# Kernel tuning notes

Measured on AMD Instinct MI355X. Metric: run time of the kernel, lower is better.

## Reference

```python
import jax, jax.numpy as jnp
import numpy as np

HEAD_DIM = 64
N_HEADS = 32
N_KV_HEADS = 8
ROPE_THETA = 10000.0
NEG_INF = -1e9


def _rope_cos_sin(position_ids, head_dim, dtype):
    # position_ids: [b, s] int -> cos/sin [b, s, head_dim]
    inv_freq = 1.0 / (ROPE_THETA ** (jnp.arange(0, head_dim, 2, dtype=jnp.float32) / head_dim))
    freqs = position_ids.astype(jnp.float32)[..., None] * inv_freq  # [b, s, d/2]
    emb = jnp.concatenate([freqs, freqs], axis=-1)                  # [b, s, d]
    return jnp.cos(emb).astype(dtype), jnp.sin(emb).astype(dtype)


def _rotate_half(x):
    half = x.shape[-1] // 2
    return jnp.concatenate([-x[..., half:], x[..., :half]], axis=-1)


def setup_inputs() -> dict:
    key = jax.random.key(0)
    ks = jax.random.split(key, 6)
    b, s, din = 2, 2048, 4096  # din = 2 * hidden_size
    hidden_states = jax.random.normal(ks[0], (b, s, din), dtype=jnp.float32)
    # additive causal mask [b, 1, q, kv]
    causal = jnp.tril(jnp.ones((s, s), dtype=bool))
    attention_mask = jnp.where(causal, 0.0, NEG_INF).astype(jnp.float32)
    attention_mask = jnp.broadcast_to(attention_mask[None, None], (b, 1, s, s))
    position_ids = jnp.broadcast_to(jnp.arange(s, dtype=jnp.int32)[None], (b, s))
    scale = 0.02
    Wq = jax.random.normal(ks[1], (din, N_HEADS * HEAD_DIM), dtype=jnp.float32) * scale
    Wk = jax.random.normal(ks[2], (din, N_KV_HEADS * HEAD_DIM), dtype=jnp.float32) * scale
    Wv = jax.random.normal(ks[3], (din, N_KV_HEADS * HEAD_DIM), dtype=jnp.float32) * scale
    Wo = jax.random.normal(ks[4], (N_HEADS * HEAD_DIM, din // 2), dtype=jnp.float32) * scale
    return {"hidden_states": hidden_states, "attention_mask": attention_mask,
            "position_ids": position_ids, "Wq": Wq, "Wk": Wk, "Wv": Wv, "Wo": Wo}


def reference(hidden_states, attention_mask, position_ids, Wq, Wk, Wv, Wo):
    b, s, _ = hidden_states.shape
    g = N_HEADS // N_KV_HEADS  # GQA group size
    q = (hidden_states @ Wq).reshape(b, s, N_HEADS, HEAD_DIM).transpose(0, 2, 1, 3)      # [b,h,s,d]
    k = (hidden_states @ Wk).reshape(b, s, N_KV_HEADS, HEAD_DIM).transpose(0, 2, 1, 3)   # [b,kh,s,d]
    v = (hidden_states @ Wv).reshape(b, s, N_KV_HEADS, HEAD_DIM).transpose(0, 2, 1, 3)
    cos, sin = _rope_cos_sin(position_ids, HEAD_DIM, q.dtype)  # [b,s,d]
    cos, sin = cos[:, None], sin[:, None]                      # [b,1,s,d]
    q = q * cos + _rotate_half(q) * sin
    k = k * cos + _rotate_half(k) * sin
    # GQA: group query heads instead of materializing repeated K/V
    qg = q.reshape(b, N_KV_HEADS, g, s, HEAD_DIM)
    scores = jnp.einsum('bhgqd,bhkd->bhgqk', qg, k) / jnp.sqrt(jnp.float32(HEAD_DIM))
    scores = scores + attention_mask[:, :, None]               # broadcast over kv-head, group
    probs = jax.nn.softmax(scores.astype(jnp.float32), axis=-1).astype(q.dtype)
    out = jnp.einsum('bhgqk,bhkd->bhgqd', probs, v)            # [b,kh,g,s,d]
    out = out.reshape(b, N_HEADS, s, HEAD_DIM).transpose(0, 2, 1, 3).reshape(b, s, N_HEADS * HEAD_DIM)
    return out @ Wo
```

## Files before the change

### kernel.cpp

```cpp
#include <hip/hip_runtime.h>
#include <hip/hip_bf16.h>
#include <cstdint>
#include <cstddef>

typedef __attribute__((ext_vector_type(4))) float floatx4;
typedef __attribute__((ext_vector_type(8))) short shortx8;

typedef __attribute__((address_space(1))) void gvoid;
typedef __attribute__((address_space(3))) void lvoid;

__device__ inline __hip_bfloat16 f2b(float x) { return __float2bfloat16(x); }
__device__ inline float b2f(__hip_bfloat16 x) { return __bfloat162float(x); }
__device__ inline unsigned cvt_pk_bf16(float lo, float hi) {
  unsigned r;
  asm("v_cvt_pk_bf16_f32 %0, %1, %2" : "=v"(r) : "v"(lo), "v"(hi));
  return r;
}
__device__ inline unsigned vmov(unsigned a) {
  unsigned r; asm("v_mov_b32 %0, %1" : "=v"(r) : "v"(a)); return r;
}
__device__ inline void plswap16(unsigned &a, unsigned &b) {
  asm("v_permlane16_swap_b32 %0, %1" : "+v"(a), "+v"(b));
}
__device__ inline void plswap32(unsigned &a, unsigned &b) {
  asm("v_permlane32_swap_b32 %0, %1" : "+v"(a), "+v"(b));
}
__device__ inline float red4_sum(float v) {
  unsigned a = __float_as_uint(v), b = vmov(a);
  plswap16(a, b);
  float s = __uint_as_float(a) + __uint_as_float(b);
  a = __float_as_uint(s); b = vmov(a);
  plswap32(a, b);
  return __uint_as_float(a) + __uint_as_float(b);
}

template <typename T> __device__ inline T cvt_out(float x);
template <> __device__ inline float cvt_out<float>(float x) { return x; }
template <> __device__ inline __hip_bfloat16 cvt_out<__hip_bfloat16>(float x) { return __float2bfloat16(x); }

__global__ void cvt_f32_bf16(const float* __restrict__ in, __hip_bfloat16* __restrict__ out, int n) {
  int i = (blockIdx.x * blockDim.x + threadIdx.x) * 4;
  if (i >= n) return;
  float4 v = *(const float4*)(in + i);
  __hip_bfloat16 o[4] = { f2b(v.x), f2b(v.y), f2b(v.z), f2b(v.w) };
  *(ushort4*)(out + i) = *(const ushort4*)o;
}

__global__ void transpose_cvt(const float* __restrict__ in, __hip_bfloat16* __restrict__ out, int K, int N) {
  __shared__ float tile[32][33];
  int n0 = blockIdx.x * 32, k0 = blockIdx.y * 32;
  int tx = threadIdx.x, ty = threadIdx.y;
#pragma unroll
  for (int i = 0; i < 4; i++)
    tile[ty + i * 8][tx] = in[(size_t)(k0 + ty + i * 8) * N + n0 + tx];
  __syncthreads();
#pragma unroll
  for (int i = 0; i < 4; i++)
    out[(size_t)(n0 + ty + i * 8) * K + k0 + tx] = f2b(tile[tx][ty + i * 8]);
}

template <typename OutT>
__global__ __launch_bounds__(256) void gemm_bt(
    const __hip_bfloat16* __restrict__ A,
    const __hip_bfloat16* __restrict__ Bt,
    OutT* __restrict__ C, int M, int N, int K) {
  __shared__ short lA[128 * 32];
  __shared__ short lB[128 * 32];
  const int m0 = blockIdx.x * 128, n0 = blockIdx.y * 128;
  const int t = threadIdx.x;
  const int l = t & 63;
  const int w = t >> 6;
  const int wm = (w & 1) * 64, wn = (w >> 1) * 64;
  const int lr = l & 15, lq = l >> 4;
  floatx4 acc[4][4] = {};

  for (int kt = 0; kt < K; kt += 32) {
    __syncthreads();
#pragma unroll
    for (int j = 0; j < 2; j++) {
      int flat = j * 2048 + t * 8;
      const __hip_bfloat16* srcA = A + (size_t)(m0 + (flat >> 5)) * K + kt + (flat & 31);
      __builtin_amdgcn_global_load_lds((gvoid*)srcA, (lvoid*)&lA[flat], 16, 0, 0);
      const __hip_bfloat16* srcB = Bt + (size_t)(n0 + (flat >> 5)) * K + kt + (flat & 31);
      __builtin_amdgcn_global_load_lds((gvoid*)srcB, (lvoid*)&lB[flat], 16, 0, 0);
    }
    __syncthreads();
    shortx8 af[4], bfr[4];
#pragma unroll
    for (int mi = 0; mi < 4; mi++)
      af[mi] = *(const shortx8*)&lA[(wm + mi * 16 + lr) * 32 + lq * 8];
#pragma unroll
    for (int ni = 0; ni < 4; ni++)
      bfr[ni] = *(const shortx8*)&lB[(wn + ni * 16 + lr) * 32 + lq * 8];
#pragma unroll
    for (int mi = 0; mi < 4; mi++)
#pragma unroll
      for (int ni = 0; ni < 4; ni++)
        acc[mi][ni] = __builtin_amdgcn_mfma_f32_16x16x32_bf16(af[mi], bfr[ni], acc[mi][ni], 0, 0, 0);
  }
#pragma unroll
  for (int mi = 0; mi < 4; mi++)
#pragma unroll
    for (int ni = 0; ni < 4; ni++) {
      int row = m0 + wm + mi * 16 + lq * 4;
      int col = n0 + wn + ni * 16 + lr;
#pragma unroll
      for (int r = 0; r < 4; r++)
        C[(size_t)(row + r) * N + col] = cvt_out<OutT>(acc[mi][ni][r]);
    }
}

__global__ void rope_kernel(__hip_bfloat16* __restrict__ q, int stride, float scale) {
  int i = threadIdx.x;
  int row = blockIdx.x * 8 + threadIdx.y;
  int head = blockIdx.y;
  int pos = row & 2047;
  float freq = (float)pos * exp2f(-(float)i * (13.287712379549449f / 32.0f));
  float s = sinf(freq), c = cosf(freq);
  __hip_bfloat16* p = q + (size_t)row * stride + head * 64 + i;
  float x1 = b2f(p[0]), x2 = b2f(p[32]);
  p[0]  = f2b((x1 * c - x2 * s) * scale);
  p[32] = f2b((x2 * c + x1 * s) * scale);
}

__global__ void v_transpose(const __hip_bfloat16* __restrict__ QKV, __hip_bfloat16* __restrict__ Vt) {
  __shared__ __hip_bfloat16 tile[32][33];
  int bkvh = blockIdx.z;
  int s0 = blockIdx.x * 32, d0 = blockIdx.y * 32;
  int b = bkvh >> 3, kvh = bkvh & 7;
  int tx = threadIdx.x, ty = threadIdx.y;
#pragma unroll
  for (int i = 0; i < 4; i++)
    tile[ty + i * 8][tx] = QKV[(size_t)(b * 2048 + s0 + ty + i * 8) * 3072 + 2560 + kvh * 64 + d0 + tx];
  __syncthreads();
#pragma unroll
  for (int i = 0; i < 4; i++)
    Vt[((size_t)(bkvh * 64 + d0 + ty + i * 8) << 11) + s0 + tx] = tile[tx][ty + i * 8];
}

__global__ __launch_bounds__(256, 3) void attn_kernel(
    const __hip_bfloat16* __restrict__ Qp,
    const __hip_bfloat16* __restrict__ Kp,
    const __hip_bfloat16* __restrict__ Vt,
    __hip_bfloat16* __restrict__ O) {
  __shared__ __align__(16) short lK[2][64 * 64];
  __shared__ __align__(16) short lV[2][64 * 64];
  const int h = blockIdx.y, b = blockIdx.z;
  const int ia = ((int)blockIdx.x + (h & 15) + ((h >> 4) << 3) + (b << 2)) & 15;
  const int ib = 31 - ia;
  const int kvh = h >> 2;
  const int t = threadIdx.x, w = t >> 6, l = t & 63;
  const int lr = l & 15, lq = l >> 4;
  const int swz = lr & 7;

  const int q0A = ia * 64 + w * 16;
  const int q0B = ib * 64 + w * 16;
  const __hip_bfloat16* qpA = Qp + (size_t)(b * 2048 + q0A + lr) * 3072 + h * 64 + lq * 8;
  const __hip_bfloat16* qpB = Qp + (size_t)(b * 2048 + q0B + lr) * 3072 + h * 64 + lq * 8;
  shortx8 qfA0 = *(const shortx8*)(qpA);
  shortx8 qfA1 = *(const shortx8*)(qpA + 32);
  shortx8 qfB0 = *(const shortx8*)(qpB);
  shortx8 qfB1 = *(const shortx8*)(qpB + 32);

  const int srow = t >> 3, schunk = t & 7;
  const int swzch = schunk ^ (srow & 7);
  const __hip_bfloat16* ksrc = Kp + (size_t)(b * 2048 + srow) * 3072 + kvh * 64 + swzch * 8;
  const __hip_bfloat16* vsrc = Vt + ((size_t)((b * 8 + kvh) * 64 + srow) << 11) + swzch * 8;

  floatx4 oA[4] = {}, oB[4] = {};
  float sumA = 0.f, sumB = 0.f;

  const int KT = 32 - ia;

  auto stage = [&](int sbuf, int kt2) {
#pragma unroll
    for (int j = 0; j < 2; j++) {
      __builtin_amdgcn_global_load_lds((gvoid*)(ksrc + (size_t)(kt2 * 64 + j * 32) * 3072),
                                       (lvoid*)&lK[sbuf][w * 512 + j * 2048], 16, 0, 0);
      __builtin_amdgcn_global_load_lds((gvoid*)(vsrc + (size_t)(j * 32) * 2048 + kt2 * 64),
                                       (lvoid*)&lV[sbuf][w * 512 + j * 2048], 16, 0, 0);
    }
  };

  stage(0, 0);

  for (int kt = 0; kt < KT; kt++) {
    const int buf = kt & 1;
    __syncthreads();
    if (kt + 1 < KT) stage(buf ^ 1, kt + 1);
    const bool doA = (kt <= ia);

    floatx4 sA[4] = {}, sB[4] = {};
    __builtin_amdgcn_s_setprio(1);
#pragma unroll
    for (int mi = 0; mi < 4; mi++) {
      const short* kr = &lK[buf][(mi * 16 + lr) * 64];
      shortx8 kf0 = *(const shortx8*)(kr + ((lq ^ swz) << 3));
      shortx8 kf1 = *(const shortx8*)(kr + (((4 + lq) ^ swz) << 3));
      if (doA) {
        sA[mi] = __builtin_amdgcn_mfma_f32_16x16x32_bf16(kf0, qfA0, sA[mi], 0, 0, 0);
        sA[mi] = __builtin_amdgcn_mfma_f32_16x16x32_bf16(kf1, qfA1, sA[mi], 0, 0, 0);
      }
      sB[mi] = __builtin_amdgcn_mfma_f32_16x16x32_bf16(kf0, qfB0, sB[mi], 0, 0, 0);
      sB[mi] = __builtin_amdgcn_mfma_f32_16x16x32_bf16(kf1, qfB1, sB[mi], 0, 0, 0);
    }
    __builtin_amdgcn_s_setprio(0);

    shortx8 pA0, pA1, pB0, pB1;

    if (doA) {
      if (kt == ia) {
#pragma unroll
        for (int mi = 0; mi < 4; mi++)
#pragma unroll
          for (int r = 0; r < 4; r++)
            if (mi * 16 + lq * 4 + r > w * 16 + lr) sA[mi][r] = -3e8f;
      }
      float rs = 0.f;
#pragma unroll
      for (int mi = 0; mi < 4; mi++) {
        float p0 = exp2f(sA[mi][0]), p1 = exp2f(sA[mi][1]);
        float p2 = exp2f(sA[mi][2]), p3 = exp2f(sA[mi][3]);
        sA[mi][0] = p0; sA[mi][1] = p1; sA[mi][2] = p2; sA[mi][3] = p3;
        rs += (p0 + p1) + (p2 + p3);
      }
      sumA += rs;
      unsigned Wm[4][2];
#pragma unroll
      for (int mi = 0; mi < 4; mi++) {
        Wm[mi][0] = cvt_pk_bf16(sA[mi][0], sA[mi][1]);
        Wm[mi][1] = cvt_pk_bf16(sA[mi][2], sA[mi][3]);
      }
      unsigned x0 = Wm[0][0], y0 = Wm[1][0]; plswap32(x0, y0); plswap16(x0, y0);
      unsigned x1 = Wm[0][1], y1 = Wm[1][1]; plswap32(x1, y1); plswap16(x1, y1);
      uint4 t0{x0, x1, y0, y1}; pA0 = *(const shortx8*)&t0;
      unsigned x2 = Wm[2][0], y2 = Wm[3][0]; plswap32(x2, y2); plswap16(x2, y2);
      unsigned x3 = Wm[2][1], y3 = Wm[3][1]; plswap32(x3, y3); plswap16(x3, y3);
      uint4 t1{x2, x3, y2, y3}; pA1 = *(const shortx8*)&t1;
    }

    {
      if (kt == KT - 1) {
#pragma unroll
        for (int mi = 0; mi < 4; mi++)
#pragma unroll
          for (int r = 0; r < 4; r++)
            if (mi * 16 + lq * 4 + r > w * 16 + lr) sB[mi][r] = -3e8f;
      }
      float rs = 0.f;
#pragma unroll
      for (int mi = 0; mi < 4; mi++) {
        float p0 = exp2f(sB[mi][0]), p1 = exp2f(sB[mi][1]);
        float p2 = exp2f(sB[mi][2]), p3 = exp2f(sB[mi][3]);
        sB[mi][0] = p0; sB[mi][1] = p1; sB[mi][2] = p2; sB[mi][3] = p3;
        rs += (p0 + p1) + (p2 + p3);
      }
      sumB += rs;
      unsigned Wm[4][2];
#pragma unroll
      for (int mi = 0; mi < 4; mi++) {
        Wm[mi][0] = cvt_pk_bf16(sB[mi][0], sB[mi][1]);
        Wm[mi][1] = cvt_pk_bf16(sB[mi][2], sB[mi][3]);
      }
      unsigned x0 = Wm[0][0], y0 = Wm[1][0]; plswap32(x0, y0); plswap16(x0, y0);
      unsigned x1 = Wm[0][1], y1 = Wm[1][1]; plswap32(x1, y1); plswap16(x1, y1);
      uint4 t0{x0, x1, y0, y1}; pB0 = *(const shortx8*)&t0;
      unsigned x2 = Wm[2][0], y2 = Wm[3][0]; plswap32(x2, y2); plswap16(x2, y2);
      unsigned x3 = Wm[2][1], y3 = Wm[3][1]; plswap32(x3, y3); plswap16(x3, y3);
      uint4 t1{x2, x3, y2, y3}; pB1 = *(const shortx8*)&t1;
    }

    __builtin_amdgcn_s_setprio(1);
#pragma unroll
    for (int mi = 0; mi < 4; mi++) {
      const short* vr = &lV[buf][(mi * 16 + lr) * 64];
      shortx8 vf0 = *(const shortx8*)(vr + ((lq ^ swz) << 3));
      shortx8 vf1 = *(const shortx8*)(vr + (((4 + lq) ^ swz) << 3));
      if (doA) {
        floatx4 o = oA[mi];
        o = __builtin_amdgcn_mfma_f32_16x16x32_bf16(vf0, pA0, o, 0, 0, 0);
        o = __builtin_amdgcn_mfma_f32_16x16x32_bf16(vf1, pA1, o, 0, 0, 0);
        oA[mi] = o;
      }
      floatx4 o2 = oB[mi];
      o2 = __builtin_amdgcn_mfma_f32_16x16x32_bf16(vf0, pB0, o2, 0, 0, 0);
      o2 = __builtin_amdgcn_mfma_f32_16x16x32_bf16(vf1, pB1, o2, 0, 0, 0);
      oB[mi] = o2;
    }
    __builtin_amdgcn_s_setprio(0);
  }

  const float livA = 1.f / red4_sum(sumA), livB = 1.f / red4_sum(sumB);
  __hip_bfloat16* obase = O + (size_t)(b * 2048 + q0A + lr) * 2048 + h * 64 + lq * 4;
#pragma unroll
  for (int mi = 0; mi < 4; mi++) {
    uint2 pk;
    pk.x = cvt_pk_bf16(oA[mi][0] * livA, oA[mi][1] * livA);
    pk.y = cvt_pk_bf16(oA[mi][2] * livA, oA[mi][3] * livA);
    *(uint2*)(obase + mi * 16) = pk;
  }
  __hip_bfloat16* obase2 = O + (size_t)(b * 2048 + q0B + lr) * 2048 + h * 64 + lq * 4;
#pragma unroll
  for (int mi = 0; mi < 4; mi++) {
    uint2 pk;
    pk.x = cvt_pk_bf16(oB[mi][0] * livB, oB[mi][1] * livB);
    pk.y = cvt_pk_bf16(oB[mi][2] * livB, oB[mi][3] * livB);
    *(uint2*)(obase2 + mi * 16) = pk;
  }
}

extern "C" void kernel_launch(void* const* d_in, const int* in_sizes, int n_in,
                              void* d_out, int out_size, void* d_ws, size_t ws_size,
                              hipStream_t stream) {
  (void)in_sizes; (void)n_in; (void)out_size; (void)ws_size;
  const float* hs = (const float*)d_in[0];
  const float* Wq = (const float*)d_in[3];
  const float* Wk = (const float*)d_in[4];
  const float* Wv = (const float*)d_in[5];
  const float* Wo = (const float*)d_in[6];
  float* out = (float*)d_out;

  char* p = (char*)d_ws;
  auto alloc = [&](size_t elts) { __hip_bfloat16* r = (__hip_bfloat16*)p; p += elts * 2; return r; };
  __hip_bfloat16* Xb   = alloc(4096ull * 4096);
  __hip_bfloat16* Wt   = alloc(3072ull * 4096);
  __hip_bfloat16* Wot  = alloc(2048ull * 2048);
  __hip_bfloat16* QKVb = alloc(4096ull * 3072);
  __hip_bfloat16* Vtb  = alloc(2ull * 8 * 64 * 2048);
  __hip_bfloat16* Ab   = alloc(4096ull * 2048);

  cvt_f32_bf16<<<16384, 256, 0, stream>>>(hs, Xb, 4096 * 4096);
  transpose_cvt<<<dim3(64, 128), dim3(32, 8), 0, stream>>>(Wq, Wt, 4096, 2048);
  transpose_cvt<<<dim3(16, 128), dim3(32, 8), 0, stream>>>(Wk, Wt + 2048ull * 4096, 4096, 512);
  transpose_cvt<<<dim3(16, 128), dim3(32, 8), 0, stream>>>(Wv, Wt + 2560ull * 4096, 4096, 512);
  transpose_cvt<<<dim3(64, 64), dim3(32, 8), 0, stream>>>(Wo, Wot, 2048, 2048);

  gemm_bt<__hip_bfloat16><<<dim3(32, 24), 256, 0, stream>>>(Xb, Wt, QKVb, 4096, 3072, 4096);

  rope_kernel<<<dim3(512, 32), dim3(32, 8), 0, stream>>>(QKVb, 3072, 0.18033688011112042f);
  rope_kernel<<<dim3(512, 8), dim3(32, 8), 0, stream>>>(QKVb + 2048, 3072, 1.0f);
  v_transpose<<<dim3(64, 2, 16), dim3(32, 8), 0, stream>>>(QKVb, Vtb);

  attn_kernel<<<dim3(16, 32, 2), 256, 0, stream>>>(QKVb, QKVb + 2048, Vtb, Ab);

  gemm_bt<float><<<dim3(32, 16), 256, 0, stream>>>(Ab, Wot, out, 4096, 2048, 2048);
}
```

Before: 492.4 us.

## Double-buffer GEMM LDS tiles with K=64 steps and XOR-swizzled layout

Rewrites the bf16 GEMM used for the QKV and output projections. K-tiles grow to 64, the LDS buffers are doubled so the next tile's global-to-LDS load overlaps the current tile's MFMAs, and LDS columns are XOR-swizzled to avoid bank conflicts. It also drops one barrier per iteration and raises wave priority around the MFMA block. LDS use grows to 64 KB per block, which may limit occupancy despite the launch bound of 2.

```diff
diff --git a/kernel.cpp b/kernel.cpp
--- a/kernel.cpp
+++ b/kernel.cpp
@@ -60,12 +60,12 @@
 }
 
 template <typename OutT>
-__global__ __launch_bounds__(256) void gemm_bt(
+__global__ __launch_bounds__(256, 2) void gemm_bt64(
     const __hip_bfloat16* __restrict__ A,
     const __hip_bfloat16* __restrict__ Bt,
     OutT* __restrict__ C, int M, int N, int K) {
-  __shared__ short lA[128 * 32];
-  __shared__ short lB[128 * 32];
+  __shared__ __align__(16) short lA[2][128 * 64];
+  __shared__ __align__(16) short lB[2][128 * 64];
   const int m0 = blockIdx.x * 128, n0 = blockIdx.y * 128;
   const int t = threadIdx.x;
   const int l = t & 63;
@@ -74,29 +74,48 @@
   const int lr = l & 15, lq = l >> 4;
   floatx4 acc[4][4] = {};
 
-  for (int kt = 0; kt < K; kt += 32) {
+  const int srow = t >> 3;
+  const int sc = (t & 7) ^ (srow & 7);
+  const __hip_bfloat16* aSrc = A + (size_t)(m0 + srow) * K + sc * 8;
+  const __hip_bfloat16* bSrc = Bt + (size_t)(n0 + srow) * K + sc * 8;
+
+  auto stage = [&](int sbuf, int kt) {
+#pragma unroll
+    for (int j = 0; j < 4; j++) {
+      __builtin_amdgcn_global_load_lds((gvoid*)(aSrc + (size_t)(j * 32) * K + kt),
+                                       (lvoid*)&lA[sbuf][t * 8 + j * 2048], 16, 0, 0);
+      __builtin_amdgcn_global_load_lds((gvoid*)(bSrc + (size_t)(j * 32) * K + kt),
+                                       (lvoid*)&lB[sbuf][t * 8 + j * 2048], 16, 0, 0);
+    }
+  };
+
+  stage(0, 0);
+  int buf = 0;
+  for (int kt = 0; kt < K; kt += 64) {
     __syncthreads();
-#pragma unroll
-    for (int j = 0; j < 2; j++) {
-      int flat = j * 2048 + t * 8;
-      const __hip_bfloat16* srcA = A + (size_t)(m0 + (flat >> 5)) * K + kt + (flat & 31);
-      __builtin_amdgcn_global_load_lds((gvoid*)srcA, (lvoid*)&lA[flat], 16, 0, 0);
-      const __hip_bfloat16* srcB = Bt + (size_t)(n0 + (flat >> 5)) * K + kt + (flat & 31);
-      __builtin_amdgcn_global_load_lds((gvoid*)srcB, (lvoid*)&lB[flat], 16, 0, 0);
-    }
-    __syncthreads();
-    shortx8 af[4], bfr[4];
-#pragma unroll
-    for (int mi = 0; mi < 4; mi++)
-      af[mi] = *(const shortx8*)&lA[(wm + mi * 16 + lr) * 32 + lq * 8];
-#pragma unroll
-    for (int ni = 0; ni < 4; ni++)
-      bfr[ni] = *(const shortx8*)&lB[(wn + ni * 16 + lr) * 32 + lq * 8];
-#pragma unroll
-    for (int mi = 0; mi < 4; mi++)
-#pragma unroll
-      for (int ni = 0; ni < 4; ni++)
-        acc[mi][ni] = __builtin_amdgcn_mfma_f32_16x16x32_bf16(af[mi], bfr[ni], acc[mi][ni], 0, 0, 0);
+    if (kt + 64 < K) stage(buf ^ 1, kt + 64);
+    __builtin_amdgcn_s_setprio(1);
+#pragma unroll
+    for (int kk = 0; kk < 2; kk++) {
+      shortx8 af[4], bfr[4];
+#pragma unroll
+      for (int mi = 0; mi < 4; mi++) {
+        int row = wm + mi * 16 + lr;
+        af[mi] = *(const shortx8*)&lA[buf][row * 64 + (((kk * 4 + lq) ^ (row & 7)) << 3)];
+      }
+#pragma unroll
+      for (int ni = 0; ni < 4; ni++) {
+        int row = wn + ni * 16 + lr;
+        bfr[ni] = *(const shortx8*)&lB[buf][row * 64 + (((kk * 4 + lq) ^ (row & 7)) << 3)];
+      }
+#pragma unroll
+      for (int mi = 0; mi < 4; mi++)
+#pragma unroll
+        for (int ni = 0; ni < 4; ni++)
+          acc[mi][ni] = __builtin_amdgcn_mfma_f32_16x16x32_bf16(af[mi], bfr[ni], acc[mi][ni], 0, 0, 0);
+    }
+    __builtin_amdgcn_s_setprio(0);
+    buf ^= 1;
   }
 #pragma unroll
   for (int mi = 0; mi < 4; mi++)
@@ -335,7 +354,7 @@
   transpose_cvt<<<dim3(16, 128), dim3(32, 8), 0, stream>>>(Wv, Wt + 2560ull * 4096, 4096, 512);
   transpose_cvt<<<dim3(64, 64), dim3(32, 8), 0, stream>>>(Wo, Wot, 2048, 2048);
 
-  gemm_bt<__hip_bfloat16><<<dim3(32, 24), 256, 0, stream>>>(Xb, Wt, QKVb, 4096, 3072, 4096);
+  gemm_bt64<__hip_bfloat16><<<dim3(32, 24), 256, 0, stream>>>(Xb, Wt, QKVb, 4096, 3072, 4096);
 
   rope_kernel<<<dim3(512, 32), dim3(32, 8), 0, stream>>>(QKVb, 3072, 0.18033688011112042f);
   rope_kernel<<<dim3(512, 8), dim3(32, 8), 0, stream>>>(QKVb + 2048, 3072, 1.0f);
@@ -343,5 +362,5 @@
 
   attn_kernel<<<dim3(16, 32, 2), 256, 0, stream>>>(QKVb, QKVb + 2048, Vtb, Ab);
 
-  gemm_bt<float><<<dim3(32, 16), 256, 0, stream>>>(Ab, Wot, out, 4096, 2048, 2048);
-}
+  gemm_bt64<float><<<dim3(32, 16), 256, 0, stream>>>(Ab, Wot, out, 4096, 2048, 2048);
+}
```

Measured after the change: 478.5 us. -2.8%, faster.
